# Performance work log

Measured on AMD Instinct MI355X. Metric: run time of the kernel, lower is better.

The kernel has to match this reference:

```python
import jax, jax.numpy as jnp
import numpy as np
from jax import lax


def _gaussian_1d(size=5, std=1.0):
    x = np.arange(size) - (size - 1) / 2.0
    return np.exp(-0.5 * (x / std) ** 2).astype(np.float32)  # scipy.signal.gaussian (unnormalized)


def _conv(x, w):
    # x: (N,1,H,W), w: (O,1,kh,kw), stride 1, SAME padding (matches torch padding=k//2)
    return lax.conv_general_dilated(x, w, (1, 1), 'SAME',
                                    dimension_numbers=('NCHW', 'OIHW', 'NCHW'))


def setup_inputs() -> dict:
    key = jax.random.key(0)
    img = jax.random.normal(key, (8, 1, 1024, 1024), dtype=jnp.float32)

    g = _gaussian_1d(5, 1.0)
    gauss_h = jnp.asarray(g.reshape(1, 1, 1, 5))
    gauss_v = jnp.asarray(g.reshape(1, 1, 5, 1))

    sob = np.array([[1, 0, -1], [2, 0, -2], [1, 0, -1]], dtype=np.float32)
    sobel_h = jnp.asarray(sob.reshape(1, 1, 3, 3))
    sobel_v = jnp.asarray(sob.T.reshape(1, 1, 3, 3))

    f0 = np.array([[0, 0, 0], [0, 1, -1], [0, 0, 0]], dtype=np.float32)
    f45 = np.array([[0, 0, 0], [0, 1, 0], [0, 0, -1]], dtype=np.float32)
    f90 = np.array([[0, 0, 0], [0, 1, 0], [0, -1, 0]], dtype=np.float32)
    f135 = np.array([[0, 0, 0], [0, 1, 0], [-1, 0, 0]], dtype=np.float32)
    f180 = np.array([[0, 0, 0], [-1, 1, 0], [0, 0, 0]], dtype=np.float32)
    f225 = np.array([[-1, 0, 0], [0, 1, 0], [0, 0, 0]], dtype=np.float32)
    f270 = np.array([[0, -1, 0], [0, 1, 0], [0, 0, 0]], dtype=np.float32)
    f315 = np.array([[0, 0, -1], [0, 1, 0], [0, 0, 0]], dtype=np.float32)
    dir_w = jnp.asarray(np.stack([f0, f45, f90, f135, f180, f225, f270, f315])[:, None])  # (8,1,3,3)

    return {"img": img, "gauss_h": gauss_h, "gauss_v": gauss_v,
            "sobel_h": sobel_h, "sobel_v": sobel_v, "dir_w": dir_w}


def reference(img, gauss_h, gauss_v, sobel_h, sobel_v, dir_w):
    THRESHOLD = 2.0
    # separable gaussian blur
    blurred = _conv(_conv(img, gauss_h), gauss_v)  # (N,1,H,W)
    # sobel gradients
    grad_x = _conv(blurred, sobel_h)
    grad_y = _conv(blurred, sobel_v)
    grad_mag = jnp.sqrt(grad_x ** 2 + grad_y ** 2)  # (N,1,H,W)
    # orientation quantized to multiples of 45 deg in [0, 360]
    grad_orientation = jnp.arctan2(grad_y, grad_x) * (180.0 / 3.14159) + 180.0
    grad_orientation = jnp.round(grad_orientation / 45.0) * 45.0
    # directional NMS (vectorized replacement of the batch-looped gather)
    all_filtered = _conv(grad_mag, dir_w)  # (N,8,H,W)
    idx_pos = (jnp.round(grad_orientation / 45.0).astype(jnp.int32)) % 8  # (N,1,H,W)
    idx_neg = (idx_pos + 4) % 8
    sel_pos = jnp.take_along_axis(all_filtered, idx_pos, axis=1)  # (N,1,H,W)
    sel_neg = jnp.take_along_axis(all_filtered, idx_neg, axis=1)
    is_max = jnp.minimum(sel_pos, sel_neg) > 0.0
    thin_edges = jnp.where(is_max, grad_mag, 0.0)
    thresholded = jnp.where(thin_edges < THRESHOLD, 0.0, thin_edges)  # computed but unused, as in source
    del thresholded
    early_threshold = jnp.where(grad_mag < THRESHOLD, 0.0, grad_mag)
    return early_threshold
```

## Files before the change

### kernel.cpp

```cpp
#include <hip/hip_runtime.h>
#include <math.h>


#define H_IMG 1024
#define W_IMG 1024
#define W4 (W_IMG / 4)
#define R 8

__global__ __launch_bounds__(256) void canny_stream(
    const float* __restrict__ img,
    const float* __restrict__ gauss,
    float* __restrict__ out)
{
    const int j  = threadIdx.x;
    const int y0 = blockIdx.x * R;
    const int b  = blockIdx.y;

    const float g0 = gauss[0], g1 = gauss[1], g2 = gauss[2];
    const float* __restrict__ imgb = img + (size_t)b * (H_IMG * W_IMG);
    float* __restrict__ outb       = out + (size_t)b * (H_IMG * W_IMG);
    const int xc = 4 * j;

    float hb[5][6];
    float bl[3][6];

    #pragma unroll
    for (int it = 0; it < R + 6; ++it) {
        const int ry = y0 - 3 + it;
        float* h = hb[it % 5];
        if (ry >= 0 && ry < H_IMG) {
            const float* p = imgb + ry * W_IMG + xc;
            float4 A = make_float4(0.f, 0.f, 0.f, 0.f);
            float4 C = make_float4(0.f, 0.f, 0.f, 0.f);
            if (j > 0)      A = *(const float4*)(p - 4);
            float4 B = *(const float4*)(p);
            if (j < W4 - 1) C = *(const float4*)(p + 4);
            h[0] = g0 * (A.y + B.y) + g1 * (A.z + B.x) + g2 * A.w;
            h[1] = g0 * (A.z + B.z) + g1 * (A.w + B.y) + g2 * B.x;
            h[2] = g0 * (A.w + B.w) + g1 * (B.x + B.z) + g2 * B.y;
            h[3] = g0 * (B.x + C.x) + g1 * (B.y + B.w) + g2 * B.z;
            h[4] = g0 * (B.y + C.y) + g1 * (B.z + C.x) + g2 * B.w;
            h[5] = g0 * (B.z + C.z) + g1 * (B.w + C.y) + g2 * C.x;
        } else {
            #pragma unroll
            for (int k = 0; k < 6; ++k) h[k] = 0.0f;
        }

        if (it >= 4) {
            const int by = ry - 2;
            float* o = bl[(it - 4) % 3];
            if (by >= 0 && by < H_IMG) {
                const float* h0 = hb[(it - 4) % 5];
                const float* h1 = hb[(it - 3) % 5];
                const float* h2 = hb[(it - 2) % 5];
                const float* h3 = hb[(it - 1) % 5];
                const float* h4 = hb[(it    ) % 5];
                #pragma unroll
                for (int k = 0; k < 6; ++k)
                    o[k] = g0 * (h0[k] + h4[k]) + g1 * (h1[k] + h3[k]) + g2 * h2[k];
                if (j == 0)      o[0] = 0.0f;
                if (j == W4 - 1) o[5] = 0.0f;
            } else {
                #pragma unroll
                for (int k = 0; k < 6; ++k) o[k] = 0.0f;
            }
        }

        if (it >= 6) {
            const int oy = ry - 3;
            const float* T  = bl[(it - 6) % 3];
            const float* M  = bl[(it - 5) % 3];
            const float* Bo = bl[(it - 4) % 3];
            float4 o4;
            float* po = (float*)&o4;
            #pragma unroll
            for (int k = 0; k < 4; ++k) {
                float gx = (T[k] - T[k + 2]) + 2.0f * (M[k] - M[k + 2]) + (Bo[k] - Bo[k + 2]);
                float gy = (T[k] + 2.0f * T[k + 1] + T[k + 2])
                         - (Bo[k] + 2.0f * Bo[k + 1] + Bo[k + 2]);
                float mag = sqrtf(gx * gx + gy * gy);
                po[k] = (mag < 2.0f) ? 0.0f : mag;
            }
            *(float4*)(outb + oy * W_IMG + xc) = o4;
        }
    }
}

extern "C" void kernel_launch(void* const* d_in, const int* in_sizes, int n_in,
                              void* d_out, int out_size, void* d_ws, size_t ws_size,
                              hipStream_t stream) {
    const float* img   = (const float*)d_in[0];
    const float* gauss = (const float*)d_in[1];
    float* out = (float*)d_out;
    const int N = in_sizes[0] / (H_IMG * W_IMG);

    dim3 grid(H_IMG / R, N);
    canny_stream<<<grid, 256, 0, stream>>>(img, gauss, out);
}
```

Before: 100.9 us.

## Batch unconditional row loads and shrink per-block output rows to four

Replaces the streaming rolling-buffer loop with a direct scheme. Each block loads a 10-row window in two batches of five clamped, unconditional float4 loads, so many loads are in flight before any compute. Out-of-range rows and image edges are handled by multiplicative masks and selects instead of branches. Output rows per block drop from 8 to 4, doubling the grid for more parallelism, but the vertical halo overhead per output row goes up and more redundant input is read.

```diff
diff --git a/kernel.cpp b/kernel.cpp
--- a/kernel.cpp
+++ b/kernel.cpp
@@ -5,84 +5,85 @@
 #define H_IMG 1024
 #define W_IMG 1024
 #define W4 (W_IMG / 4)
-#define R 8
+#define P 4
+#define WIN (P + 6)
 
-__global__ __launch_bounds__(256) void canny_stream(
+__global__ __launch_bounds__(256) void canny_direct(
     const float* __restrict__ img,
     const float* __restrict__ gauss,
     float* __restrict__ out)
 {
-    const int j  = threadIdx.x;
-    const int y0 = blockIdx.x * R;
-    const int b  = blockIdx.y;
+    const int j   = threadIdx.x;
+    const int xc  = 4 * j;
+    const int oy0 = blockIdx.x * P;
+    const int b   = blockIdx.y;
 
     const float g0 = gauss[0], g1 = gauss[1], g2 = gauss[2];
     const float* __restrict__ imgb = img + (size_t)b * (H_IMG * W_IMG);
     float* __restrict__ outb       = out + (size_t)b * (H_IMG * W_IMG);
-    const int xc = 4 * j;
+    const float4 zero4 = make_float4(0.f, 0.f, 0.f, 0.f);
 
-    float hb[5][6];
-    float bl[3][6];
+    float t[WIN][6];
 
     #pragma unroll
-    for (int it = 0; it < R + 6; ++it) {
-        const int ry = y0 - 3 + it;
-        float* h = hb[it % 5];
-        if (ry >= 0 && ry < H_IMG) {
-            const float* p = imgb + ry * W_IMG + xc;
-            float4 A = make_float4(0.f, 0.f, 0.f, 0.f);
-            float4 C = make_float4(0.f, 0.f, 0.f, 0.f);
-            if (j > 0)      A = *(const float4*)(p - 4);
-            float4 B = *(const float4*)(p);
-            if (j < W4 - 1) C = *(const float4*)(p + 4);
-            h[0] = g0 * (A.y + B.y) + g1 * (A.z + B.x) + g2 * A.w;
-            h[1] = g0 * (A.z + B.z) + g1 * (A.w + B.y) + g2 * B.x;
-            h[2] = g0 * (A.w + B.w) + g1 * (B.x + B.z) + g2 * B.y;
-            h[3] = g0 * (B.x + C.x) + g1 * (B.y + B.w) + g2 * B.z;
-            h[4] = g0 * (B.y + C.y) + g1 * (B.z + C.x) + g2 * B.w;
-            h[5] = g0 * (B.z + C.z) + g1 * (B.w + C.y) + g2 * C.x;
-        } else {
-            #pragma unroll
-            for (int k = 0; k < 6; ++k) h[k] = 0.0f;
+    for (int ph = 0; ph < 2; ++ph) {
+        float4 A[5], B[5], C[5];
+        #pragma unroll
+        for (int i = 0; i < 5; ++i) {
+            const int r  = oy0 - 3 + ph * 5 + i;
+            const int rc = r < 0 ? 0 : (r > H_IMG - 1 ? H_IMG - 1 : r);
+            const float* p = imgb + rc * W_IMG + xc;
+            A[i] = *(const float4*)(j > 0      ? p - 4 : p);
+            B[i] = *(const float4*)p;
+            C[i] = *(const float4*)(j < W4 - 1 ? p + 4 : p);
         }
+        #pragma unroll
+        for (int i = 0; i < 5; ++i) {
+            const int r = oy0 - 3 + ph * 5 + i;
+            const float m = (r >= 0 && r < H_IMG) ? 1.0f : 0.0f;
+            float4 Ai = A[i], Bi = B[i], Ci = C[i];
+            if (j == 0)      Ai = zero4;
+            if (j == W4 - 1) Ci = zero4;
+            float* h = t[ph * 5 + i];
+            h[0] = m * (g0 * (Ai.y + Bi.y) + g1 * (Ai.z + Bi.x) + g2 * Ai.w);
+            h[1] = m * (g0 * (Ai.z + Bi.z) + g1 * (Ai.w + Bi.y) + g2 * Bi.x);
+            h[2] = m * (g0 * (Ai.w + Bi.w) + g1 * (Bi.x + Bi.z) + g2 * Bi.y);
+            h[3] = m * (g0 * (Bi.x + Ci.x) + g1 * (Bi.y + Bi.w) + g2 * Bi.z);
+            h[4] = m * (g0 * (Bi.y + Ci.y) + g1 * (Bi.z + Ci.x) + g2 * Bi.w);
+            h[5] = m * (g0 * (Bi.z + Ci.z) + g1 * (Bi.w + Ci.y) + g2 * Ci.x);
+        }
+    }
 
-        if (it >= 4) {
-            const int by = ry - 2;
-            float* o = bl[(it - 4) % 3];
-            if (by >= 0 && by < H_IMG) {
-                const float* h0 = hb[(it - 4) % 5];
-                const float* h1 = hb[(it - 3) % 5];
-                const float* h2 = hb[(it - 2) % 5];
-                const float* h3 = hb[(it - 1) % 5];
-                const float* h4 = hb[(it    ) % 5];
-                #pragma unroll
-                for (int k = 0; k < 6; ++k)
-                    o[k] = g0 * (h0[k] + h4[k]) + g1 * (h1[k] + h3[k]) + g2 * h2[k];
-                if (j == 0)      o[0] = 0.0f;
-                if (j == W4 - 1) o[5] = 0.0f;
-            } else {
-                #pragma unroll
-                for (int k = 0; k < 6; ++k) o[k] = 0.0f;
-            }
+    float bl[P + 2][6];
+    #pragma unroll
+    for (int k = 0; k < P + 2; ++k) {
+        const int r = oy0 - 1 + k;
+        const float m = (r >= 0 && r < H_IMG) ? 1.0f : 0.0f;
+        #pragma unroll
+        for (int c = 0; c < 6; ++c)
+            bl[k][c] = m * (g0 * (t[k][c] + t[k + 4][c])
+                          + g1 * (t[k + 1][c] + t[k + 3][c])
+                          + g2 *  t[k + 2][c]);
+        if (j == 0)      bl[k][0] = 0.0f;
+        if (j == W4 - 1) bl[k][5] = 0.0f;
+    }
+
+    #pragma unroll
+    for (int mrow = 0; mrow < P; ++mrow) {
+        const float* T  = bl[mrow];
+        const float* M  = bl[mrow + 1];
+        const float* Bo = bl[mrow + 2];
+        float4 o4;
+        float* po = (float*)&o4;
+        #pragma unroll
+        for (int k = 0; k < 4; ++k) {
+            float gx = (T[k] - T[k + 2]) + 2.0f * (M[k] - M[k + 2]) + (Bo[k] - Bo[k + 2]);
+            float gy = (T[k] + 2.0f * T[k + 1] + T[k + 2])
+                     - (Bo[k] + 2.0f * Bo[k + 1] + Bo[k + 2]);
+            float mag = sqrtf(gx * gx + gy * gy);
+            po[k] = (mag < 2.0f) ? 0.0f : mag;
         }
-
-        if (it >= 6) {
-            const int oy = ry - 3;
-            const float* T  = bl[(it - 6) % 3];
-            const float* M  = bl[(it - 5) % 3];
-            const float* Bo = bl[(it - 4) % 3];
-            float4 o4;
-            float* po = (float*)&o4;
-            #pragma unroll
-            for (int k = 0; k < 4; ++k) {
-                float gx = (T[k] - T[k + 2]) + 2.0f * (M[k] - M[k + 2]) + (Bo[k] - Bo[k + 2]);
-                float gy = (T[k] + 2.0f * T[k + 1] + T[k + 2])
-                         - (Bo[k] + 2.0f * Bo[k + 1] + Bo[k + 2]);
-                float mag = sqrtf(gx * gx + gy * gy);
-                po[k] = (mag < 2.0f) ? 0.0f : mag;
-            }
-            *(float4*)(outb + oy * W_IMG + xc) = o4;
-        }
+        *(float4*)(outb + (oy0 + mrow) * W_IMG + xc) = o4;
     }
 }
 
@@ -94,6 +95,6 @@
     float* out = (float*)d_out;
     const int N = in_sizes[0] / (H_IMG * W_IMG);
 
-    dim3 grid(H_IMG / R, N);
-    canny_stream<<<grid, 256, 0, stream>>>(img, gauss, out);
+    dim3 grid(H_IMG / P, N);
+    canny_direct<<<grid, 256, 0, stream>>>(img, gauss, out);
 }
```

New measurement: 105.1 us. 1.04x slower.
